# Kernel optimization log

Hardware: AMD Instinct MI355X
Metric: run time of the kernel (lower is better)

Reference implementation:

```python
import jax, jax.numpy as jnp
import numpy as np

NX, T_IN, T_OUT = 256, 16, 128
STATE, PSIZE = 1, 4
WIDTH, DEPTH = 128, 4
BATCH = 4


def _build_edges(B):
    # Faithful vectorized replica of create_graph_structure (incl. the
    # batch-mixing .view(2,-1) on a (B,2,E) tensor).
    ng = NX * T_OUT
    # spatial edges: loops t outer, i inner, fwd/bwd interleaved
    a = (np.arange(T_OUT)[:, None] * NX + np.arange(NX - 1)[None, :]).reshape(-1)
    sp = np.stack([np.stack([a, a + 1], 1), np.stack([a + 1, a], 1)], 1).reshape(-1, 2)
    # temporal edges: loops x outer, t inner, fwd/bwd interleaved
    b = (np.arange(NX)[:, None] + np.arange(T_OUT - 1)[None, :] * NX).reshape(-1)
    tp = np.stack([np.stack([b, b + NX], 1), np.stack([b + NX, b], 1)], 1).reshape(-1, 2)
    base = np.concatenate([sp, tp], 0).T  # (2, E)
    ei = base[None, :, :] + (np.arange(B) * ng)[:, None, None]  # (B, 2, E)
    return ei.reshape(2, -1)  # row-major flatten, same as torch .view(2, -1)


def _layernorm(x, g, b, eps=1e-5):
    mu = x.mean(-1, keepdims=True)
    var = x.var(-1, keepdims=True)  # biased, same as torch LayerNorm
    return (x - mu) * jax.lax.rsqrt(var + eps) * g + b


def setup_inputs():
    key = jax.random.key(0)
    ks = jax.random.split(key, 8)
    d_in = STATE + PSIZE + 2
    return {
        "u0": jax.random.normal(ks[0], (BATCH, NX, T_IN, STATE), jnp.float32),
        "P": jax.random.normal(ks[1], (BATCH, PSIZE), jnp.float32),
        "W_in": jax.random.normal(ks[2], (d_in, WIDTH), jnp.float32) / np.sqrt(d_in),
        "b_in": jnp.zeros((WIDTH,), jnp.float32),
        "Wg": jax.random.normal(ks[3], (DEPTH, WIDTH, WIDTH), jnp.float32) / np.sqrt(WIDTH),
        "bg": jnp.zeros((DEPTH, WIDTH), jnp.float32),
        "gamma": jnp.ones((DEPTH, WIDTH), jnp.float32),
        "beta": jnp.zeros((DEPTH, WIDTH), jnp.float32),
        "W_out": jax.random.normal(ks[4], (WIDTH, STATE), jnp.float32) / np.sqrt(WIDTH),
        "b_out": jnp.zeros((STATE,), jnp.float32),
    }


def reference(u0, P, W_in, b_in, Wg, bg, gamma, beta, W_out, b_out):
    B = u0.shape[0]
    ng = NX * T_OUT
    N = B * ng

    ei = _build_edges(B)
    loops = np.arange(N)
    src = jnp.asarray(np.concatenate([ei[0], loops]))  # GCN adds self-loops
    dst = jnp.asarray(np.concatenate([ei[1], loops]))
    deg = jnp.zeros((N,), jnp.float32).at[dst].add(1.0)  # in-degree incl. self-loop
    dis = jnp.where(deg > 0, jax.lax.rsqrt(deg), 0.0)
    norm = (dis[src] * dis[dst])[:, None]  # symmetric GCN normalization

    # grid features flattened x-major (matches meshgrid 'ij' reshape(-1,1))
    xg = jnp.repeat(jnp.linspace(0.0, 1.0, NX), T_OUT)[None, :, None]
    tg = jnp.tile(jnp.linspace(0.0, 1.0, T_OUT), NX)[None, :, None]

    # bilinear resize (nx_in, T_in) -> (NX, T_OUT), align_corners=False semantics
    u0i = jax.image.resize(u0, (B, NX, T_OUT, STATE), "bilinear").reshape(B, ng, STATE)
    Pex = jnp.broadcast_to(P[:, None, :], (B, ng, PSIZE))
    feat = jnp.concatenate(
        [u0i, Pex, jnp.broadcast_to(xg, (B, ng, 1)), jnp.broadcast_to(tg, (B, ng, 1))], -1
    )
    x = (feat @ W_in + b_in).reshape(N, WIDTH)

    for l in range(DEPTH):
        h = x @ Wg[l]                      # GCNConv linear
        msg = h[src] * norm                # gather + normalize
        h = jax.ops.segment_sum(msg, dst, num_segments=N) + bg[l]  # scatter-add
        h = _layernorm(h, gamma[l], beta[l])
        x = jax.nn.relu(h + x)             # residual then ReLU

    out = x @ W_out + b_out
    return out.reshape(B, NX, T_OUT, STATE)
```

## Files before the change

### kernel.cpp

```cpp
#include <hip/hip_runtime.h>
#include <hip/hip_bf16.h>

#define NXX 256
#define NG 32768
#define WID 128
#define STRW 68

typedef short bf16x8 __attribute__((ext_vector_type(8)));
typedef float f32x4 __attribute__((ext_vector_type(4)));

__device__ __forceinline__ unsigned short rne_bf16(float x) {
    unsigned int u = __float_as_uint(x);
    return (unsigned short)((u + 0x7fffu + ((u >> 16) & 1u)) >> 16);
}

__global__ __launch_bounds__(64) void prep_kernel(
    const float* __restrict__ Wg, unsigned short* __restrict__ Bfrag) {
    const int e  = blockIdx.x;
    const int lv = threadIdx.x;
    const int l  = e >> 5;
    const int kc = (e >> 3) & 3;
    const int nt = e & 7;
    const int n  = nt * 16 + (lv & 15);
    const int kb = kc * 32 + ((lv >> 4) << 3);
#pragma unroll
    for (int j = 0; j < 8; ++j) {
        float v = Wg[(size_t)l * 16384 + (size_t)(kb + j) * WID + n];
        Bfrag[(size_t)e * 512 + lv * 8 + j] = rne_bf16(v);
    }
}

__device__ __forceinline__ unsigned int pack_bf2(float a, float b) {
    union { __hip_bfloat162 h2; unsigned int u; } cv;
    cv.h2 = __float22bfloat162_rn(make_float2(a, b));
    return cv.u;
}

__global__ __launch_bounds__(256) void fused_kernel(
    const float* __restrict__ u0, const float* __restrict__ P,
    const float* __restrict__ W_in, const float* __restrict__ b_in,
    const unsigned short* __restrict__ Bfrag,
    const float* __restrict__ bg, const float* __restrict__ gamma,
    const float* __restrict__ beta, const float* __restrict__ W_out,
    const float* __restrict__ b_out, float* __restrict__ out)
{
    __shared__ unsigned int XsH[8][16 * STRW];

    const int tid  = threadIdx.x;
    const int w    = tid >> 6;
    const int lane = tid & 63;
    const int l15  = lane & 15;
    const int lhi  = lane >> 4;

    const int blk  = blockIdx.x;
    const int b    = blk >> 9;
    const int ublk = (blk & 511) << 6;

    const int u  = ublk + 16 * w + l15;
    const int ix = u >> 7;
    const int t  = u & 127;

    float c1, c2;
    {
        int gi = u & 255, gt = u >> 8;
        int d  = (gi > 0) + (gi < 255) + (gt > 0) + (gt < 127);
        float deg = 2.f * (float)d + 1.f;
        c1 = 2.f * (float)d * rsqrtf(deg);
        c2 = 1.f / deg;
    }

    float featA[7], featB[7];
    {
        float s  = ((float)t + 0.5f) * 0.125f - 0.5f;
        float fs = floorf(s);
        int   t0 = (int)fs;
        float wt = s - fs;
        int t0c = t0 < 0 ? 0 : (t0 > 15 ? 15 : t0);
        int t1n = t0 + 1;
        int t1c = t1n < 0 ? 0 : (t1n > 15 ? 15 : t1n);
        const float* urA = u0 + ((size_t)b * NXX + ix) * 16;
        const float* urB = u0 + ((size_t)(b + 2) * NXX + ix) * 16;
        featA[0] = urA[t0c] * (1.f - wt) + urA[t1c] * wt;
        featB[0] = urB[t0c] * (1.f - wt) + urB[t1c] * wt;
#pragma unroll
        for (int f = 0; f < 4; ++f) {
            featA[1 + f] = P[b * 4 + f];
            featB[1 + f] = P[(b + 2) * 4 + f];
        }
        featA[5] = featB[5] = (float)ix * (1.f / 255.f);
        featA[6] = featB[6] = (float)t  * (1.f / 127.f);
    }

    float xr0[8][4], xr1[8][4];
#pragma unroll
    for (int nt = 0; nt < 8; ++nt) {
        const int c = nt * 16 + 4 * lhi;
        float4 bi4 = *(const float4*)(b_in + c);
        float4 wf[7];
#pragma unroll
        for (int f = 0; f < 7; ++f) wf[f] = *(const float4*)(W_in + f * WID + c);
#pragma unroll
        for (int r = 0; r < 4; ++r) {
            float a0 = ((const float*)&bi4)[r];
            float a1 = a0;
#pragma unroll
            for (int f = 0; f < 7; ++f) {
                float wv = ((const float*)&wf[f])[r];
                a0 = fmaf(featA[f], wv, a0);
                a1 = fmaf(featB[f], wv, a1);
            }
            xr0[nt][r] = a0;
            xr1[nt][r] = a1;
        }
    }

    unsigned int* Hrow0 = &XsH[2 * w][l15 * STRW];
    unsigned int* Hrow1 = &XsH[2 * w + 1][l15 * STRW];

    for (int l = 0; l < 4; ++l) {
#pragma unroll
        for (int nt = 0; nt < 8; ++nt) {
            unsigned int p0 = pack_bf2(xr0[nt][0], xr0[nt][1]);
            unsigned int p1 = pack_bf2(xr0[nt][2], xr0[nt][3]);
            *(uint2*)(Hrow0 + 8 * nt + 2 * lhi) = make_uint2(p0, p1);
            unsigned int q0 = pack_bf2(xr1[nt][0], xr1[nt][1]);
            unsigned int q1 = pack_bf2(xr1[nt][2], xr1[nt][3]);
            *(uint2*)(Hrow1 + 8 * nt + 2 * lhi) = make_uint2(q0, q1);
        }

        f32x4 acc0[8], acc1[8];
#pragma unroll
        for (int nt = 0; nt < 8; ++nt) {
            acc0[nt] = (f32x4){0.f, 0.f, 0.f, 0.f};
            acc1[nt] = (f32x4){0.f, 0.f, 0.f, 0.f};
        }
        const unsigned short* bp = Bfrag + (size_t)l * 16384 + lane * 8;
#pragma unroll
        for (int kc = 0; kc < 4; ++kc) {
            bf16x8 x0 = *(const bf16x8*)(Hrow0 + 16 * kc + 4 * lhi);
            bf16x8 x1 = *(const bf16x8*)(Hrow1 + 16 * kc + 4 * lhi);
#pragma unroll
            for (int nt = 0; nt < 8; ++nt) {
                bf16x8 bh = *(const bf16x8*)(bp + (kc * 8 + nt) * 512);
                acc0[nt] = __builtin_amdgcn_mfma_f32_16x16x32_bf16(bh, x0, acc0[nt], 0, 0, 0);
                acc1[nt] = __builtin_amdgcn_mfma_f32_16x16x32_bf16(bh, x1, acc1[nt], 0, 0, 0);
            }
        }

        float s0 = 0.f, q0 = 0.f, s1 = 0.f, q1 = 0.f;
#pragma unroll
        for (int nt = 0; nt < 8; ++nt) {
            float4 bg4 = *(const float4*)(bg + l * WID + nt * 16 + 4 * lhi);
#pragma unroll
            for (int r = 0; r < 4; ++r) {
                float bgr = ((const float*)&bg4)[r];
                float h0 = acc0[nt][r];
                float h1 = acc1[nt][r];
                float a0 = h0 + bgr;
                float a1 = fmaf(c1, h0, fmaf(c2, h1, bgr));
                acc0[nt][r] = a0;
                acc1[nt][r] = a1;
                s0 += a0;  q0 = fmaf(a0, a0, q0);
                s1 += a1;  q1 = fmaf(a1, a1, q1);
            }
        }
        s0 += __shfl_xor(s0, 16);  q0 += __shfl_xor(q0, 16);
        s1 += __shfl_xor(s1, 16);  q1 += __shfl_xor(q1, 16);
        s0 += __shfl_xor(s0, 32);  q0 += __shfl_xor(q0, 32);
        s1 += __shfl_xor(s1, 32);  q1 += __shfl_xor(q1, 32);
        float mu0 = s0 * (1.f / 128.f);
        float mu1 = s1 * (1.f / 128.f);
        float rs0 = rsqrtf(q0 * (1.f / 128.f) - mu0 * mu0 + 1e-5f);
        float rs1 = rsqrtf(q1 * (1.f / 128.f) - mu1 * mu1 + 1e-5f);
#pragma unroll
        for (int nt = 0; nt < 8; ++nt) {
            const int c = nt * 16 + 4 * lhi;
            float4 g4 = *(const float4*)(gamma + l * WID + c);
            float4 e4 = *(const float4*)(beta  + l * WID + c);
#pragma unroll
            for (int r = 0; r < 4; ++r) {
                float gv = ((const float*)&g4)[r];
                float ev = ((const float*)&e4)[r];
                float n0 = fmaf((acc0[nt][r] - mu0) * rs0, gv, ev);
                float n1 = fmaf((acc1[nt][r] - mu1) * rs1, gv, ev);
                xr0[nt][r] = fmaxf(n0 + xr0[nt][r], 0.f);
                xr1[nt][r] = fmaxf(n1 + xr1[nt][r], 0.f);
            }
        }
    }

    float p0 = 0.f, p1 = 0.f;
#pragma unroll
    for (int nt = 0; nt < 8; ++nt) {
        float4 wo4 = *(const float4*)(W_out + nt * 16 + 4 * lhi);
#pragma unroll
        for (int r = 0; r < 4; ++r) {
            float wv = ((const float*)&wo4)[r];
            p0 = fmaf(xr0[nt][r], wv, p0);
            p1 = fmaf(xr1[nt][r], wv, p1);
        }
    }
    p0 += __shfl_xor(p0, 16);  p1 += __shfl_xor(p1, 16);
    p0 += __shfl_xor(p0, 32);  p1 += __shfl_xor(p1, 32);
    if (lhi == 0) {
        float bo = b_out[0];
        out[(size_t)b * NG + u]       = p0 + bo;
        out[(size_t)(b + 2) * NG + u] = p1 + bo;
    }
}

extern "C" void kernel_launch(void* const* d_in, const int* in_sizes, int n_in,
                              void* d_out, int out_size, void* d_ws, size_t ws_size,
                              hipStream_t stream) {
    const float* u0    = (const float*)d_in[0];
    const float* P     = (const float*)d_in[1];
    const float* W_in  = (const float*)d_in[2];
    const float* b_in  = (const float*)d_in[3];
    const float* Wg    = (const float*)d_in[4];
    const float* bg    = (const float*)d_in[5];
    const float* gamma = (const float*)d_in[6];
    const float* beta  = (const float*)d_in[7];
    const float* W_out = (const float*)d_in[8];
    const float* b_out = (const float*)d_in[9];

    unsigned short* Bfrag = (unsigned short*)d_ws;

    prep_kernel<<<128, 64, 0, stream>>>(Wg, Bfrag);
    fused_kernel<<<1024, 256, 0, stream>>>(
        u0, P, W_in, b_in, Bfrag, bg, gamma, beta, W_out, b_out, (float*)d_out);
}
```

Baseline: 62.40 us.

## Feed MFMA B-operand directly from registers by permuting the K order of the weights

Removes the per-layer LDS round trip (bf16 pack, store to shared, reload as MFMA fragments) by building the activation fragment directly from accumulator-layout registers. To make that valid, the prep kernel permutes the K ordering of the weight fragments so each lane's 8 K-values match the channels it already holds. This drops LDS traffic and shared memory use, which may help occupancy, at the cost of relying on the permuted K mapping being consistent in both kernels.

```diff
diff --git a/kernel.cpp b/kernel.cpp
--- a/kernel.cpp
+++ b/kernel.cpp
@@ -4,10 +4,10 @@
 #define NXX 256
 #define NG 32768
 #define WID 128
-#define STRW 68
 
 typedef short bf16x8 __attribute__((ext_vector_type(8)));
 typedef float f32x4 __attribute__((ext_vector_type(4)));
+typedef unsigned int u32x4 __attribute__((ext_vector_type(4)));
 
 __device__ __forceinline__ unsigned short rne_bf16(float x) {
     unsigned int u = __float_as_uint(x);
@@ -22,10 +22,11 @@
     const int kc = (e >> 3) & 3;
     const int nt = e & 7;
     const int n  = nt * 16 + (lv & 15);
-    const int kb = kc * 32 + ((lv >> 4) << 3);
+    const int g  = lv >> 4;
 #pragma unroll
     for (int j = 0; j < 8; ++j) {
-        float v = Wg[(size_t)l * 16384 + (size_t)(kb + j) * WID + n];
+        const int ch = kc * 32 + ((j >> 2) << 4) + (g << 2) + (j & 3);
+        float v = Wg[(size_t)l * 16384 + (size_t)ch * WID + n];
         Bfrag[(size_t)e * 512 + lv * 8 + j] = rne_bf16(v);
     }
 }
@@ -35,6 +36,8 @@
     cv.h2 = __float22bfloat162_rn(make_float2(a, b));
     return cv.u;
 }
+
+union fragu { bf16x8 f; u32x4 u; };
 
 __global__ __launch_bounds__(256) void fused_kernel(
     const float* __restrict__ u0, const float* __restrict__ P,
@@ -44,8 +47,6 @@
     const float* __restrict__ beta, const float* __restrict__ W_out,
     const float* __restrict__ b_out, float* __restrict__ out)
 {
-    __shared__ unsigned int XsH[8][16 * STRW];
-
     const int tid  = threadIdx.x;
     const int w    = tid >> 6;
     const int lane = tid & 63;
@@ -114,20 +115,7 @@
         }
     }
 
-    unsigned int* Hrow0 = &XsH[2 * w][l15 * STRW];
-    unsigned int* Hrow1 = &XsH[2 * w + 1][l15 * STRW];
-
     for (int l = 0; l < 4; ++l) {
-#pragma unroll
-        for (int nt = 0; nt < 8; ++nt) {
-            unsigned int p0 = pack_bf2(xr0[nt][0], xr0[nt][1]);
-            unsigned int p1 = pack_bf2(xr0[nt][2], xr0[nt][3]);
-            *(uint2*)(Hrow0 + 8 * nt + 2 * lhi) = make_uint2(p0, p1);
-            unsigned int q0 = pack_bf2(xr1[nt][0], xr1[nt][1]);
-            unsigned int q1 = pack_bf2(xr1[nt][2], xr1[nt][3]);
-            *(uint2*)(Hrow1 + 8 * nt + 2 * lhi) = make_uint2(q0, q1);
-        }
-
         f32x4 acc0[8], acc1[8];
 #pragma unroll
         for (int nt = 0; nt < 8; ++nt) {
@@ -137,13 +125,20 @@
         const unsigned short* bp = Bfrag + (size_t)l * 16384 + lane * 8;
 #pragma unroll
         for (int kc = 0; kc < 4; ++kc) {
-            bf16x8 x0 = *(const bf16x8*)(Hrow0 + 16 * kc + 4 * lhi);
-            bf16x8 x1 = *(const bf16x8*)(Hrow1 + 16 * kc + 4 * lhi);
+            fragu x0f, x1f;
+            x0f.u = (u32x4){pack_bf2(xr0[2 * kc][0],     xr0[2 * kc][1]),
+                            pack_bf2(xr0[2 * kc][2],     xr0[2 * kc][3]),
+                            pack_bf2(xr0[2 * kc + 1][0], xr0[2 * kc + 1][1]),
+                            pack_bf2(xr0[2 * kc + 1][2], xr0[2 * kc + 1][3])};
+            x1f.u = (u32x4){pack_bf2(xr1[2 * kc][0],     xr1[2 * kc][1]),
+                            pack_bf2(xr1[2 * kc][2],     xr1[2 * kc][3]),
+                            pack_bf2(xr1[2 * kc + 1][0], xr1[2 * kc + 1][1]),
+                            pack_bf2(xr1[2 * kc + 1][2], xr1[2 * kc + 1][3])};
 #pragma unroll
             for (int nt = 0; nt < 8; ++nt) {
                 bf16x8 bh = *(const bf16x8*)(bp + (kc * 8 + nt) * 512);
-                acc0[nt] = __builtin_amdgcn_mfma_f32_16x16x32_bf16(bh, x0, acc0[nt], 0, 0, 0);
-                acc1[nt] = __builtin_amdgcn_mfma_f32_16x16x32_bf16(bh, x1, acc1[nt], 0, 0, 0);
+                acc0[nt] = __builtin_amdgcn_mfma_f32_16x16x32_bf16(bh, x0f.f, acc0[nt], 0, 0, 0);
+                acc1[nt] = __builtin_amdgcn_mfma_f32_16x16x32_bf16(bh, x1f.f, acc1[nt], 0, 0, 0);
             }
         }
 
```

Result: faster. 55.30 us (median of 2 runs) (-11.4%).
